# Performance work log

Measured on AMD Instinct MI355X. Metric: run time of the kernel, lower is better.

The kernel has to match this reference:

```python
import jax, jax.numpy as jnp
import numpy as np
import math

B, T, N, C = 16, 24, 207, 64
E = 16   # embedding_dim
L = 3    # num_layers
NH = 4   # temporal attention heads
HD = C // NH
HOR = 12 # horizon


def _ln(x, w, b, eps=1e-5):
    m = x.mean(-1, keepdims=True)
    v = ((x - m) ** 2).mean(-1, keepdims=True)
    return (x - m) / jnp.sqrt(v + eps) * w + b


def setup_inputs():
    ks = iter(jax.random.split(jax.random.key(0), 64))
    def g(shape, s=0.1):
        return jax.random.normal(next(ks), shape, dtype=jnp.float32) * s
    inp = {}
    inp['x'] = jax.random.normal(next(ks), (B, T, N, 4), dtype=jnp.float32)
    adj = (jax.random.uniform(next(ks), (N, N)) < 0.3).astype(jnp.float32)
    inp['static_adj'] = jnp.maximum(adj, jnp.eye(N, dtype=jnp.float32))  # self-loops: no all-zero rows
    inp['node_embedding'] = g((N, E), 1.0)
    for nm in ['hour', 'day', 'weekend']:
        inp[nm + '_w'] = g((E, 1)); inp[nm + '_b'] = g((E,))
    inp['in_w'] = g((C, 1 + 4 * E)); inp['in_b'] = g((C,))
    C8 = C // 8
    inp['sa_qw'] = g((L, C8, C)); inp['sa_qb'] = g((L, C8))
    inp['sa_kw'] = g((L, C8, C)); inp['sa_kb'] = g((L, C8))
    inp['sa_vw'] = g((L, C, C)); inp['sa_vb'] = g((L, C))
    for nm in ['ta_q', 'ta_k', 'ta_v', 'ta_o']:
        inp[nm + 'w'] = g((L, C, C)); inp[nm + 'b'] = g((L, C))
    inp['ln1_w'] = jnp.ones((L, C)); inp['ln1_b'] = jnp.zeros((L, C))
    inp['ln2_w'] = jnp.ones((L, C)); inp['ln2_b'] = jnp.zeros((L, C))
    inp['ffn_w1'] = g((L, 4 * C, C)); inp['ffn_b1'] = g((L, 4 * C))
    inp['ffn_w2'] = g((L, C, 4 * C)); inp['ffn_b2'] = g((L, C))
    inp['gru_wih'] = g((2, 3 * C, C)); inp['gru_whh'] = g((2, 3 * C, C))
    inp['gru_bih'] = g((2, 3 * C)); inp['gru_bhh'] = g((2, 3 * C))
    inp['pred_w'] = g((HOR, C * T), 0.02); inp['pred_b'] = g((HOR,))
    return inp


def _forward(x, static_adj, node_embedding, hour_w, hour_b, day_w, day_b, weekend_w, weekend_b, in_w, in_b, sa_qw, sa_qb, sa_kw, sa_kb, sa_vw, sa_vb, ta_qw, ta_qb, ta_kw, ta_kb, ta_vw, ta_vb, ta_ow, ta_ob, ln1_w, ln1_b, ln2_w, ln2_b, ffn_w1, ffn_b1, ffn_w2, ffn_b2, gru_wih, gru_whh, gru_bih, gru_bhh, pred_w, pred_b):
    # eval mode: dropout = identity, no input perturbation
    flow = x[..., :1]
    hour = x[..., 1:2]; weekend = x[..., 2:3]; day = x[..., 3:4]
    node_emb = jnp.broadcast_to(node_embedding[None, None], (B, T, N, E))
    hour_emb = hour @ hour_w.T + hour_b
    day_emb = day @ day_w.T + day_b
    weekend_emb = weekend @ weekend_w.T + weekend_b
    h = jnp.concatenate([flow, node_emb, hour_emb, day_emb, weekend_emb], axis=-1)  # [B,T,N,65]
    h = h.transpose(0, 3, 2, 1)  # [B,F,N,T]
    h = jnp.einsum('of,bfnt->bont', in_w, h) + in_b[None, :, None, None]  # 1x1 conv -> [B,C,N,T]
    # positional encoding (added along channel/time, matching permute in torch)
    pos = jnp.arange(100, dtype=jnp.float32)[:, None]
    div = jnp.exp(jnp.arange(0, C, 2, dtype=jnp.float32) * (-math.log(10000.0) / C))
    pe = jnp.stack([jnp.sin(pos * div), jnp.cos(pos * div)], axis=-1).reshape(100, C)
    h = h + pe[:T].T[None, :, None, :]
    # F.normalize(adj, p=1, dim=-1) with eps clamp (torch default 1e-12)
    adj_norm = static_adj / jnp.maximum(jnp.abs(static_adj).sum(-1, keepdims=True), 1e-12)
    zero_mask = (adj_norm == 0)[None]  # [1,N,N]
    attn_mats = []
    sqrtC = math.sqrt(C); sqrtHD = math.sqrt(HD)
    for l in range(L):
        # ---- spatial attention (faithful dim-mixing reshapes of the original) ----
        hp = h.transpose(0, 1, 3, 2)  # [B,C,T,N]
        q = jnp.einsum('oc,bctn->botn', sa_qw[l], hp) + sa_qb[l][None, :, None, None]
        k = jnp.einsum('oc,bctn->botn', sa_kw[l], hp) + sa_kb[l][None, :, None, None]
        v = jnp.einsum('oc,bctn->botn', sa_vw[l], hp) + sa_vb[l][None, :, None, None]
        C8 = q.shape[1]
        q2 = q.reshape(B * T, C8, N).transpose(0, 2, 1)
        k2 = k.reshape(B * T, C8, N)
        v2 = v.reshape(B * T, C, N)
        attn = jax.nn.softmax(jnp.einsum('bnc,bcm->bnm', q2, k2) / sqrtC, axis=-1)
        attn = jnp.where(zero_mask, -jnp.inf, attn)
        attn = jax.nn.softmax(attn, axis=-1)
        sp = jnp.einsum('bcn,bmn->bcm', v2, attn).reshape(B, T, C, N).transpose(0, 2, 3, 1)  # [B,C,N,T]
        attn_mats.append(attn.reshape(B, T, N, N))
        h = h + sp
        h = _ln(h.transpose(0, 3, 2, 1), ln1_w[l], ln1_b[l]).transpose(0, 3, 2, 1)
        # ---- temporal attention (multi-head over time, per node) ----
        xt = h.transpose(0, 2, 3, 1)  # [B,N,T,C]
        def heads(w, b):
            return (xt @ w.T + b).reshape(B, N, T, NH, HD).transpose(0, 1, 3, 2, 4)
        tq = heads(ta_qw[l], ta_qb[l]); tk = heads(ta_kw[l], ta_kb[l]); tv = heads(ta_vw[l], ta_vb[l])
        scores = jnp.einsum('bnhtd,bnhsd->bnhts', tq, tk) / sqrtHD
        ta = jnp.einsum('bnhts,bnhsd->bnhtd', jax.nn.softmax(scores, axis=-1), tv)
        ta = ta.transpose(0, 1, 3, 2, 4).reshape(B, N, T, C) @ ta_ow[l].T + ta_ob[l]
        h = h + ta.transpose(0, 3, 1, 2)
        # ---- LN2 + FFN (residual taken post-LN2, as in the original) ----
        hl = _ln(h.transpose(0, 3, 2, 1), ln2_w[l], ln2_b[l])  # [B,T,N,C]
        ffn = jax.nn.relu(hl @ ffn_w1[l].T + ffn_b1[l]) @ ffn_w2[l].T + ffn_b2[l]
        h = (hl + ffn).transpose(0, 3, 2, 1)
    # ---- 2-layer GRU over time per (batch, node) ----
    seq = h.transpose(0, 2, 3, 1).reshape(B * N, T, C).transpose(1, 0, 2)  # [T,BN,C]
    for l in range(2):
        xp = jnp.einsum('tbc,gc->tbg', seq, gru_wih[l]) + gru_bih[l]
        whh = gru_whh[l]; bhh = gru_bhh[l]
        def step(hprev, xg):
            hg = hprev @ whh.T + bhh
            r = jax.nn.sigmoid(xg[:, :C] + hg[:, :C])
            z = jax.nn.sigmoid(xg[:, C:2 * C] + hg[:, C:2 * C])
            n = jnp.tanh(xg[:, 2 * C:] + r * hg[:, 2 * C:])
            hnew = (1 - z) * n + z * hprev
            return hnew, hnew
        _, seq = jax.lax.scan(step, jnp.zeros((B * N, C), dtype=seq.dtype), xp)
    h = seq.transpose(1, 0, 2).reshape(B, N, T, C).transpose(0, 3, 1, 2)  # [B,C,N,T]
    # ---- prediction head ----
    flat = h.transpose(0, 2, 1, 3).reshape(B * N, C * T)
    out = (flat @ pred_w.T + pred_b).reshape(B, N, HOR).transpose(0, 2, 1)  # [B,HOR,N]
    return out, attn_mats


def reference(x, static_adj, node_embedding, hour_w, hour_b, day_w, day_b, weekend_w, weekend_b, in_w, in_b, sa_qw, sa_qb, sa_kw, sa_kb, sa_vw, sa_vb, ta_qw, ta_qb, ta_kw, ta_kb, ta_vw, ta_vb, ta_ow, ta_ob, ln1_w, ln1_b, ln2_w, ln2_b, ffn_w1, ffn_b1, ffn_w2, ffn_b2, gru_wih, gru_whh, gru_bih, gru_bhh, pred_w, pred_b):
    out, attn_mats = _forward(x, static_adj, node_embedding, hour_w, hour_b, day_w, day_b, weekend_w, weekend_b, in_w, in_b, sa_qw, sa_qb, sa_kw, sa_kb, sa_vw, sa_vb, ta_qw, ta_qb, ta_kw, ta_kb, ta_vw, ta_vb, ta_ow, ta_ob, ln1_w, ln1_b, ln2_w, ln2_b, ffn_w1, ffn_b1, ffn_w2, ffn_b2, gru_wih, gru_whh, gru_bih, gru_bhh, pred_w, pred_b)
    return (out, jnp.stack(attn_mats))
```

## Files before the change

### kernel.cpp

```cpp
#include <hip/hip_runtime.h>
#include <math.h>

namespace {

constexpr int B = 16, T = 24, N = 207, C = 64, HOR = 12;
constexpr int BT = B * T;
constexpr int BN = B * N;
constexpr int P = B * T * N;
constexpr int NC = N * C;

constexpr size_t H_OFF = 0;
constexpr size_t A_OFF = 5087232;
constexpr size_t Q_OFF = A_OFF + 5087232;
constexpr size_t K_OFF = Q_OFF + 635904;
constexpr size_t B_OFF = K_OFF + 635904;
constexpr size_t WS_FLOATS = B_OFF + 20348928;

__device__ __forceinline__ float wsum(float v) {
#pragma unroll
  for (int off = 32; off; off >>= 1) v += __shfl_xor(v, off);
  return v;
}
__device__ __forceinline__ float wmax(float v) {
#pragma unroll
  for (int off = 32; off; off >>= 1) v = fmaxf(v, __shfl_xor(v, off));
  return v;
}

__global__ __launch_bounds__(256) void k_embed(
    const float* __restrict__ x, const float* __restrict__ nodee,
    const float* __restrict__ hw, const float* __restrict__ hb,
    const float* __restrict__ dw, const float* __restrict__ db,
    const float* __restrict__ ww, const float* __restrict__ wb,
    const float* __restrict__ inw, const float* __restrict__ inb,
    float* __restrict__ H) {
  int pos = blockIdx.x * 4 + (threadIdx.x >> 6);
  int c = threadIdx.x & 63;
  int n = pos % N;
  int t = (pos / N) % T;
  const float* xv = x + (size_t)pos * 4;
  float flow = xv[0], hour = xv[1], wkend = xv[2], day = xv[3];
  const float* w = inw + c * 65;
  float acc = inb[c] + w[0] * flow;
#pragma unroll
  for (int e = 0; e < 16; e++) {
    acc += w[1 + e] * nodee[n * 16 + e];
    acc += w[17 + e] * (hour * hw[e] + hb[e]);
    acc += w[33 + e] * (day * dw[e] + db[e]);
    acc += w[49 + e] * (wkend * ww[e] + wb[e]);
  }
  int i = c >> 1;
  float dv = expf((float)(2 * i) * (-9.210340371976184f / 64.0f));
  float ang = (float)t * dv;
  acc += (c & 1) ? cosf(ang) : sinf(ang);
  H[(size_t)pos * 64 + c] = acc;
}

__global__ __launch_bounds__(256) void k_spatial_qkv(
    const float* __restrict__ H, const float* __restrict__ qw,
    const float* __restrict__ qb, const float* __restrict__ kw,
    const float* __restrict__ kb, const float* __restrict__ vw,
    const float* __restrict__ vb, float* __restrict__ q, float* __restrict__ k,
    float* __restrict__ v, int l) {
  __shared__ float hs[N * 65];
  int g = blockIdx.x;
  int b = g / T, t = g % T;
  const float* Hbt = H + (size_t)g * NC;
  for (int e = threadIdx.x; e < NC; e += 256) {
    int n = e >> 6, c = e & 63;
    hs[n * 65 + c] = Hbt[e];
  }
  __syncthreads();
  qw += l * 8 * 64; qb += l * 8;
  kw += l * 8 * 64; kb += l * 8;
  vw += l * 64 * 64; vb += l * 64;
  for (int e = threadIdx.x; e < 16 * N; e += 256) {
    int o = e / N, n = e % N;
    int oo = o & 7;
    const float* W = (o < 8 ? qw : kw) + oo * 64;
    float acc = (o < 8 ? qb : kb)[oo];
#pragma unroll
    for (int c = 0; c < 64; c++) acc += W[c] * hs[n * 65 + c];
    size_t oidx = ((size_t)(b * 8 + oo) * T + t) * N + n;
    if (o < 8) q[oidx] = acc; else k[oidx] = acc;
  }
  for (int e = threadIdx.x; e < 64 * N; e += 256) {
    int o = e / N, n = e % N;
    const float* W = vw + o * 64;
    float acc = vb[o];
#pragma unroll
    for (int c = 0; c < 64; c++) acc += W[c] * hs[n * 65 + c];
    v[((size_t)(b * 64 + o) * T + t) * N + n] = acc;
  }
}

__global__ __launch_bounds__(256) void k_spatial_attn(
    const float* __restrict__ q, const float* __restrict__ k,
    const float* __restrict__ adj, float* __restrict__ attn_out) {
  __shared__ float qs[8 * 208], ks[8 * 208];
  int g = blockIdx.x;
  const float* qg = q + (size_t)g * 1656;
  const float* kg = k + (size_t)g * 1656;
  for (int e = threadIdx.x; e < 1656; e += 256) {
    int c2 = e / N, n = e % N;
    qs[c2 * 208 + n] = qg[e];
    ks[c2 * 208 + n] = kg[e];
  }
  __syncthreads();
  int wave = threadIdx.x >> 6, lane = threadIdx.x & 63;
  for (int n = wave; n < N; n += 4) {
    float s[4];
    float mx = -INFINITY;
#pragma unroll
    for (int j = 0; j < 4; j++) {
      int m = lane + 64 * j;
      float acc = -INFINITY;
      if (m < N) {
        acc = 0.f;
#pragma unroll
        for (int c2 = 0; c2 < 8; c2++) acc += qs[c2 * 208 + n] * ks[c2 * 208 + m];
        acc *= 0.125f;
      }
      s[j] = acc;
      mx = fmaxf(mx, acc);
    }
    mx = wmax(mx);
    float sum = 0.f;
#pragma unroll
    for (int j = 0; j < 4; j++) {
      int m = lane + 64 * j;
      float e = (m < N) ? expf(s[j] - mx) : 0.f;
      s[j] = e;
      sum += e;
    }
    sum = wsum(sum);
    float inv = 1.f / sum;
    float mx2 = -INFINITY;
    bool ok[4];
#pragma unroll
    for (int j = 0; j < 4; j++) {
      int m = lane + 64 * j;
      float p = s[j] * inv;
      bool valid = (m < N) && (adj[n * N + m] != 0.0f);
      ok[j] = valid;
      s[j] = p;
      if (valid) mx2 = fmaxf(mx2, p);
    }
    mx2 = wmax(mx2);
    float sum2 = 0.f;
#pragma unroll
    for (int j = 0; j < 4; j++) {
      float e = ok[j] ? expf(s[j] - mx2) : 0.f;
      s[j] = e;
      sum2 += e;
    }
    sum2 = wsum(sum2);
    float inv2 = 1.f / sum2;
    float* orow = attn_out + ((size_t)g * N + n) * N;
#pragma unroll
    for (int j = 0; j < 4; j++) {
      int m = lane + 64 * j;
      if (m < N) orow[m] = s[j] * inv2;
    }
  }
}

__global__ __launch_bounds__(256, 3) void k_spatial_apply(
    const float* __restrict__ v, const float* __restrict__ attn,
    float* __restrict__ H) {
  __shared__ float vs[64 * 207];
  int g = blockIdx.x;
  int ms = blockIdx.y;
  const float* vg = v + (size_t)g * NC;
  for (int e = threadIdx.x; e < NC; e += 256) vs[e] = vg[e];
  __syncthreads();
  int wave = threadIdx.x >> 6, lane = threadIdx.x & 63;
  const float* ag = attn + (size_t)g * (N * N);
  float* Hg = H + (size_t)g * NC;
  int mbeg = ms * 52;
  int mend = min(mbeg + 52, N);
  int m_w = mbeg + wave;
  size_t Dg = (size_t)g * (N * N);
  int p = (int)((4 - ((Dg + (size_t)m_w * N) & 3)) & 3);
  const float* ar[13];
  int mrow[13];
#pragma unroll
  for (int r = 0; r < 13; r++) {
    int m = m_w + 4 * r;
    mrow[r] = m;
    int msafe = (m < N) ? m : m - 4;
    ar[r] = ag + (size_t)msafe * N;
  }
  float acc[13];
#pragma unroll
  for (int r = 0; r < 13; r++) acc[r] = 0.f;
  const float* vrow = vs + lane * 207;
  for (int n = 0; n < p; n++) {
    float vv = vrow[n];
#pragma unroll
    for (int r = 0; r < 13; r++) acc[r] += vv * ar[r][n];
  }
  for (int n4 = 0; n4 < 51; n4++) {
    int n = p + n4 * 4;
    float v0 = vrow[n], v1 = vrow[n + 1], v2 = vrow[n + 2], v3 = vrow[n + 3];
#pragma unroll
    for (int r = 0; r < 13; r++) {
      float4 a = *(const float4*)(ar[r] + n);
      acc[r] += v0 * a.x;
      acc[r] += v1 * a.y;
      acc[r] += v2 * a.z;
      acc[r] += v3 * a.w;
    }
  }
  for (int n = p + 204; n < 207; n++) {
    float vv = vrow[n];
#pragma unroll
    for (int r = 0; r < 13; r++) acc[r] += vv * ar[r][n];
  }
#pragma unroll
  for (int r = 0; r < 13; r++) {
    int m = mrow[r];
    if (m < mend) Hg[(size_t)m * 64 + lane] += acc[r];
  }
}

__global__ __launch_bounds__(256) void k_ln1(float* __restrict__ H,
                                             const float* __restrict__ w,
                                             const float* __restrict__ b, int l) {
  int pos = blockIdx.x * 4 + (threadIdx.x >> 6);
  int c = threadIdx.x & 63;
  float xv = H[(size_t)pos * 64 + c];
  float mean = wsum(xv) * (1.f / 64.f);
  float d = xv - mean;
  float var = wsum(d * d) * (1.f / 64.f);
  H[(size_t)pos * 64 + c] = d / sqrtf(var + 1e-5f) * w[l * 64 + c] + b[l * 64 + c];
}

__global__ __launch_bounds__(256) void k_temporal(
    float* __restrict__ H, const float* __restrict__ qw,
    const float* __restrict__ qb, const float* __restrict__ kw,
    const float* __restrict__ kb, const float* __restrict__ vw,
    const float* __restrict__ vb, const float* __restrict__ ow,
    const float* __restrict__ ob, int l) {
  __shared__ float xs[24 * 66], qs[24 * 66], ks[24 * 66], vs[24 * 66];
  __shared__ float ss[96 * 25];
  __shared__ float wbuf[64 * 65];
  int bn = blockIdx.x;
  int b = bn / N, n = bn % N;
  size_t base = ((size_t)b * T * N + n) * 64;
  int lane = threadIdx.x & 63, tg = threadIdx.x >> 6;
  for (int t = tg; t < 24; t += 4) xs[t * 66 + lane] = H[base + (size_t)t * NC + lane];
  const float* Wm[4] = {qw + l * 4096, kw + l * 4096, vw + l * 4096, ow + l * 4096};
  const float* Bm[4] = {qb + l * 64, kb + l * 64, vb + l * 64, ob + l * 64};
  float* Dm[3] = {qs, ks, vs};
#pragma unroll
  for (int ph = 0; ph < 3; ph++) {
    for (int e = threadIdx.x; e < 4096; e += 256)
      wbuf[(e >> 6) * 65 + (e & 63)] = Wm[ph][e];
    __syncthreads();
    float acc[6];
    float bv = Bm[ph][lane];
#pragma unroll
    for (int i = 0; i < 6; i++) acc[i] = bv;
    for (int c = 0; c < 64; c++) {
      float wv = wbuf[lane * 65 + c];
#pragma unroll
      for (int i = 0; i < 6; i++) acc[i] += wv * xs[(tg * 6 + i) * 66 + c];
    }
    float* dst = Dm[ph];
#pragma unroll
    for (int i = 0; i < 6; i++) dst[(tg * 6 + i) * 66 + lane] = acc[i];
    __syncthreads();
  }
  for (int e = threadIdx.x; e < 2304; e += 256) {
    int u = e % 24, t = (e / 24) % 24, h = e / 576;
    float a = 0.f;
#pragma unroll
    for (int d = 0; d < 16; d++)
      a += qs[t * 66 + h * 16 + d] * ks[u * 66 + h * 16 + d];
    ss[(h * 24 + t) * 25 + u] = a * 0.25f;
  }
  __syncthreads();
  if (threadIdx.x < 96) {
    float* row = ss + threadIdx.x * 25;
    float mx = -INFINITY;
#pragma unroll
    for (int u = 0; u < 24; u++) mx = fmaxf(mx, row[u]);
    float sum = 0.f;
#pragma unroll
    for (int u = 0; u < 24; u++) {
      float e2 = expf(row[u] - mx);
      row[u] = e2;
      sum += e2;
    }
    float inv = 1.f / sum;
#pragma unroll
    for (int u = 0; u < 24; u++) row[u] *= inv;
  }
  __syncthreads();
  for (int e = threadIdx.x; e < 1536; e += 256) {
    int t = e >> 6, c = e & 63, h = c >> 4;
    float a = 0.f;
#pragma unroll
    for (int u = 0; u < 24; u++) a += ss[(h * 24 + t) * 25 + u] * vs[u * 66 + c];
    xs[t * 66 + c] = a;
  }
  __syncthreads();
  for (int e = threadIdx.x; e < 4096; e += 256)
    wbuf[(e >> 6) * 65 + (e & 63)] = Wm[3][e];
  __syncthreads();
  float acc[6];
  float bv = Bm[3][lane];
#pragma unroll
  for (int i = 0; i < 6; i++) acc[i] = bv;
  for (int cp = 0; cp < 64; cp++) {
    float wv = wbuf[lane * 65 + cp];
#pragma unroll
    for (int i = 0; i < 6; i++) acc[i] += wv * xs[(tg * 6 + i) * 66 + cp];
  }
#pragma unroll
  for (int i = 0; i < 6; i++)
    H[base + (size_t)(tg * 6 + i) * NC + lane] += acc[i];
}

__global__ __launch_bounds__(256) void k_transpose_ffn(
    const float* __restrict__ w1, const float* __restrict__ w2,
    float* __restrict__ w1t, float* __restrict__ w2q, int l) {
  int e = blockIdx.x * 256 + threadIdx.x;
  if (e < 16384) {
    int c = e >> 8, j = e & 255;
    w1t[e] = w1[l * 16384 + j * 64 + c];
  } else {
    int m = e - 16384;
    int jq = m >> 8, c = (m & 255) >> 2, kk = m & 3;
    w2q[m] = w2[l * 16384 + c * 256 + jq * 4 + kk];
  }
}

__global__ __launch_bounds__(256) void k_ffn(
    float* __restrict__ H, const float* __restrict__ lnw,
    const float* __restrict__ lnb, const float* __restrict__ w1t,
    const float* __restrict__ b1, const float* __restrict__ w2q,
    const float* __restrict__ b2, int l) {
  __shared__ float xs[24 * 66];
  __shared__ float hids[24 * 260];
  int bn = blockIdx.x;
  int b = bn / N, n = bn % N;
  size_t base = ((size_t)b * T * N + n) * 64;
  int lane = threadIdx.x & 63, tg = threadIdx.x >> 6;
  for (int t = tg; t < 24; t += 4) {
    float xv = H[base + (size_t)t * NC + lane];
    float mean = wsum(xv) * (1.f / 64.f);
    float d = xv - mean;
    float var = wsum(d * d) * (1.f / 64.f);
    xs[t * 66 + lane] = d / sqrtf(var + 1e-5f) * lnw[l * 64 + lane] + lnb[l * 64 + lane];
  }
  __syncthreads();
  int j0 = lane * 4;
  float4 b4 = *(const float4*)(b1 + l * 256 + j0);
  float a0[6], a1[6], a2[6], a3[6];
#pragma unroll
  for (int i = 0; i < 6; i++) { a0[i] = b4.x; a1[i] = b4.y; a2[i] = b4.z; a3[i] = b4.w; }
  for (int c = 0; c < 64; c++) {
    float4 w4 = *(const float4*)(w1t + c * 256 + j0);
#pragma unroll
    for (int i = 0; i < 6; i++) {
      float xv = xs[(tg * 6 + i) * 66 + c];
      a0[i] += xv * w4.x;
      a1[i] += xv * w4.y;
      a2[i] += xv * w4.z;
      a3[i] += xv * w4.w;
    }
  }
#pragma unroll
  for (int i = 0; i < 6; i++) {
    int t = tg * 6 + i;
    float4 r = make_float4(fmaxf(a0[i], 0.f), fmaxf(a1[i], 0.f),
                           fmaxf(a2[i], 0.f), fmaxf(a3[i], 0.f));
    *(float4*)(&hids[t * 260 + j0]) = r;
  }
  __syncthreads();
  const float4* w2q4 = (const float4*)w2q;
  float acc[6];
#pragma unroll
  for (int i = 0; i < 6; i++) acc[i] = 0.f;
  for (int jq = 0; jq < 64; jq++) {
    float4 w = w2q4[jq * 64 + lane];
#pragma unroll
    for (int i = 0; i < 6; i++) {
      float4 hv = *(const float4*)(&hids[(tg * 6 + i) * 260 + jq * 4]);
      acc[i] += hv.x * w.x + hv.y * w.y + hv.z * w.z + hv.w * w.w;
    }
  }
  float bias = b2[l * 64 + lane];
#pragma unroll
  for (int i = 0; i < 6; i++) {
    int t = tg * 6 + i;
    H[base + (size_t)t * NC + lane] = xs[t * 66 + lane] + bias + acc[i];
  }
}

__global__ __launch_bounds__(256) void k_gru_xp(
    const float* __restrict__ X, const float* __restrict__ wih,
    const float* __restrict__ bih, float* __restrict__ xp, int l) {
  __shared__ float ws_[192 * 65];
  __shared__ float xv[16 * 64];
  int p0 = blockIdx.x * 16;
  for (int e = threadIdx.x; e < 192 * 64; e += 256) {
    int gI = e >> 6, c = e & 63;
    ws_[gI * 65 + c] = wih[l * 12288 + e];
  }
  for (int e = threadIdx.x; e < 16 * 64; e += 256) {
    int s = e >> 6, c = e & 63;
    int p = p0 + s;
    int t = p / BN, bn = p % BN;
    float val;
    if (l == 0) {
      int b = bn / N, n = bn % N;
      val = X[(((size_t)b * T + t) * N + n) * 64 + c];
    } else {
      val = X[(size_t)p * 64 + c];
    }
    xv[e] = val;
  }
  __syncthreads();
  for (int e = threadIdx.x; e < 16 * 192; e += 256) {
    int s = e / 192, gI = e % 192;
    float acc = bih[l * 192 + gI];
#pragma unroll
    for (int c = 0; c < 64; c++) acc += xv[s * 64 + c] * ws_[gI * 65 + c];
    xp[((size_t)(p0 + s)) * 192 + gI] = acc;
  }
}

__global__ __launch_bounds__(256) void k_gru_scan(
    const float* __restrict__ xp, const float* __restrict__ whh,
    const float* __restrict__ bhh, float* __restrict__ seq_out, int l) {
  constexpr int S = 8;
  __shared__ float hprev[S][64];
  __shared__ float hg[3][S][64];
  __shared__ float xpbuf[2][S * 192];
  int bn0 = blockIdx.x * S;
  int lane = threadIdx.x & 63;
  int wv = threadIdx.x >> 6;

  float4 w4[16];
  if (wv < 3) {
    const float* wr = whh + l * 12288 + (wv * 64 + lane) * 64;
#pragma unroll
    for (int j = 0; j < 16; j++) w4[j] = *(const float4*)(wr + j * 4);
  }
  float b_r = bhh[l * 192 + lane];
  float b_z = bhh[l * 192 + 64 + lane];
  float b_n = bhh[l * 192 + 128 + lane];

  for (int e = threadIdx.x; e < S * 64; e += 256) ((float*)hprev)[e] = 0.f;
  {
    const float* src = xp + (size_t)bn0 * 192;
    for (int e = threadIdx.x; e < S * 192; e += 256) xpbuf[0][e] = src[e];
  }
  __syncthreads();

  for (int t = 0; t < T; t++) {
    int cur = t & 1;
    if (wv < 3) {
      float acc[S];
#pragma unroll
      for (int s = 0; s < S; s++) acc[s] = 0.f;
#pragma unroll
      for (int j = 0; j < 16; j++) {
        float4 w = w4[j];
#pragma unroll
        for (int s = 0; s < S; s++) {
          float4 hb = *(const float4*)(&hprev[s][j * 4]);
          acc[s] += w.x * hb.x + w.y * hb.y + w.z * hb.z + w.w * hb.w;
        }
      }
#pragma unroll
      for (int s = 0; s < S; s++) hg[wv][s][lane] = acc[s];
    } else {
      if (t + 1 < T) {
        const float* src = xp + ((size_t)(t + 1) * BN + bn0) * 192;
        float* dst = xpbuf[(t + 1) & 1];
        for (int e = lane * 4; e < S * 192; e += 256) {
          *(float4*)(dst + e) = *(const float4*)(src + e);
        }
      }
    }
    __syncthreads();
#pragma unroll
    for (int ii = 0; ii < 2; ii++) {
      int s = wv + 4 * ii;
      const float* xr = &xpbuf[cur][s * 192];
      float r = 1.f / (1.f + expf(-(xr[lane] + hg[0][s][lane] + b_r)));
      float z = 1.f / (1.f + expf(-(xr[64 + lane] + hg[1][s][lane] + b_z)));
      float nn = tanhf(xr[128 + lane] + r * (hg[2][s][lane] + b_n));
      float hp = hprev[s][lane];
      float hnew = (1.f - z) * nn + z * hp;
      hprev[s][lane] = hnew;
      seq_out[((size_t)t * BN + bn0 + s) * 64 + lane] = hnew;
    }
    __syncthreads();
  }
}

__global__ __launch_bounds__(256) void k_pred(
    const float* __restrict__ seq2, const float* __restrict__ pw,
    const float* __restrict__ pb, float* __restrict__ out) {
  __shared__ float s_[1536];
  int bn = blockIdx.x;
  int b = bn / N, n = bn % N;
  for (int e = threadIdx.x; e < 1536; e += 256) {
    int t = e >> 6, c = e & 63;
    s_[c * 24 + t] = seq2[((size_t)t * BN + bn) * 64 + c];
  }
  __syncthreads();
  int wave = threadIdx.x >> 6, lane = threadIdx.x & 63;
  for (int hor = wave; hor < 12; hor += 4) {
    const float* w = pw + hor * 1536;
    float acc = 0.f;
#pragma unroll 4
    for (int kk = lane; kk < 1536; kk += 64) acc += s_[kk] * w[kk];
    acc = wsum(acc);
    if (lane == 0) out[(size_t)b * (HOR * N) + hor * N + n] = acc + pb[hor];
  }
}

}

extern "C" void kernel_launch(void* const* d_in, const int* in_sizes, int n_in,
                              void* d_out, int out_size, void* d_ws, size_t ws_size,
                              hipStream_t stream) {
  const float* x       = (const float*)d_in[0];
  const float* adj     = (const float*)d_in[1];
  const float* nodee   = (const float*)d_in[2];
  const float* hour_w  = (const float*)d_in[3];
  const float* hour_b  = (const float*)d_in[4];
  const float* day_w   = (const float*)d_in[5];
  const float* day_b   = (const float*)d_in[6];
  const float* wk_w    = (const float*)d_in[7];
  const float* wk_b    = (const float*)d_in[8];
  const float* in_w    = (const float*)d_in[9];
  const float* in_b    = (const float*)d_in[10];
  const float* sa_qw   = (const float*)d_in[11];
  const float* sa_qb   = (const float*)d_in[12];
  const float* sa_kw   = (const float*)d_in[13];
  const float* sa_kb   = (const float*)d_in[14];
  const float* sa_vw   = (const float*)d_in[15];
  const float* sa_vb   = (const float*)d_in[16];
  const float* ta_qw   = (const float*)d_in[17];
  const float* ta_qb   = (const float*)d_in[18];
  const float* ta_kw   = (const float*)d_in[19];
  const float* ta_kb   = (const float*)d_in[20];
  const float* ta_vw   = (const float*)d_in[21];
  const float* ta_vb   = (const float*)d_in[22];
  const float* ta_ow   = (const float*)d_in[23];
  const float* ta_ob   = (const float*)d_in[24];
  const float* ln1_w   = (const float*)d_in[25];
  const float* ln1_b   = (const float*)d_in[26];
  const float* ln2_w   = (const float*)d_in[27];
  const float* ln2_b   = (const float*)d_in[28];
  const float* ffn_w1  = (const float*)d_in[29];
  const float* ffn_b1  = (const float*)d_in[30];
  const float* ffn_w2  = (const float*)d_in[31];
  const float* ffn_b2  = (const float*)d_in[32];
  const float* gru_wih = (const float*)d_in[33];
  const float* gru_whh = (const float*)d_in[34];
  const float* gru_bih = (const float*)d_in[35];
  const float* gru_bhh = (const float*)d_in[36];
  const float* pred_w  = (const float*)d_in[37];
  const float* pred_b  = (const float*)d_in[38];

  if (ws_size < WS_FLOATS * sizeof(float)) return;

  float* ws   = (float*)d_ws;
  float* H    = ws + H_OFF;
  float* bufA = ws + A_OFF;
  float* q    = ws + Q_OFF;
  float* k    = ws + K_OFF;
  float* bufB = ws + B_OFF;

  float* out       = (float*)d_out;
  float* attn_base = out + (size_t)B * HOR * N;

  float* v   = bufB;
  float* xp  = bufB;
  float* w1t = q;
  float* w2q = k;

  k_embed<<<P / 4, 256, 0, stream>>>(x, nodee, hour_w, hour_b, day_w, day_b,
                                     wk_w, wk_b, in_w, in_b, H);

  for (int l = 0; l < 3; l++) {
    float* attn_l = attn_base + (size_t)l * BT * N * N;
    k_spatial_qkv<<<BT, 256, 0, stream>>>(H, sa_qw, sa_qb, sa_kw, sa_kb, sa_vw,
                                          sa_vb, q, k, v, l);
    k_spatial_attn<<<BT, 256, 0, stream>>>(q, k, adj, attn_l);
    k_spatial_apply<<<dim3(BT, 4), 256, 0, stream>>>(v, attn_l, H);
    k_ln1<<<P / 4, 256, 0, stream>>>(H, ln1_w, ln1_b, l);
    k_temporal<<<BN, 256, 0, stream>>>(H, ta_qw, ta_qb, ta_kw, ta_kb, ta_vw,
                                       ta_vb, ta_ow, ta_ob, l);
    k_transpose_ffn<<<128, 256, 0, stream>>>(ffn_w1, ffn_w2, w1t, w2q, l);
    k_ffn<<<BN, 256, 0, stream>>>(H, ln2_w, ln2_b, w1t, ffn_b1, w2q, ffn_b2, l);
  }

  k_gru_xp<<<P / 16, 256, 0, stream>>>(H, gru_wih, gru_bih, xp, 0);
  k_gru_scan<<<BN / 8, 256, 0, stream>>>(xp, gru_whh, gru_bhh, bufA, 0);
  k_gru_xp<<<P / 16, 256, 0, stream>>>(bufA, gru_wih, gru_bih, xp, 1);
  k_gru_scan<<<BN / 8, 256, 0, stream>>>(xp, gru_whh, gru_bhh, H, 1);

  k_pred<<<BN, 256, 0, stream>>>(H, pred_w, pred_b, out);
}
```

Measured before the change: 2.397 ms.

## Fuse LayerNorm1 into temporal attention and read pre-packed weights from global

```diff
diff --git a/kernel.cpp b/kernel.cpp
--- a/kernel.cpp
+++ b/kernel.cpp
@@ -224,60 +224,59 @@
   }
 }
 
-__global__ __launch_bounds__(256) void k_ln1(float* __restrict__ H,
-                                             const float* __restrict__ w,
-                                             const float* __restrict__ b, int l) {
-  int pos = blockIdx.x * 4 + (threadIdx.x >> 6);
-  int c = threadIdx.x & 63;
-  float xv = H[(size_t)pos * 64 + c];
-  float mean = wsum(xv) * (1.f / 64.f);
-  float d = xv - mean;
-  float var = wsum(d * d) * (1.f / 64.f);
-  H[(size_t)pos * 64 + c] = d / sqrtf(var + 1e-5f) * w[l * 64 + c] + b[l * 64 + c];
-}
-
 __global__ __launch_bounds__(256) void k_temporal(
-    float* __restrict__ H, const float* __restrict__ qw,
-    const float* __restrict__ qb, const float* __restrict__ kw,
-    const float* __restrict__ kb, const float* __restrict__ vw,
-    const float* __restrict__ vb, const float* __restrict__ ow,
-    const float* __restrict__ ob, int l) {
-  __shared__ float xs[24 * 66], qs[24 * 66], ks[24 * 66], vs[24 * 66];
+    float* __restrict__ H, const float* __restrict__ taq,
+    const float* __restrict__ qb, const float* __restrict__ kb,
+    const float* __restrict__ vb, const float* __restrict__ ob,
+    const float* __restrict__ lnw, const float* __restrict__ lnb, int l) {
+  __shared__ float xs[24 * 68], qs[24 * 68], ks[24 * 68], vs[24 * 68];
   __shared__ float ss[96 * 25];
-  __shared__ float wbuf[64 * 65];
   int bn = blockIdx.x;
   int b = bn / N, n = bn % N;
   size_t base = ((size_t)b * T * N + n) * 64;
   int lane = threadIdx.x & 63, tg = threadIdx.x >> 6;
-  for (int t = tg; t < 24; t += 4) xs[t * 66 + lane] = H[base + (size_t)t * NC + lane];
-  const float* Wm[4] = {qw + l * 4096, kw + l * 4096, vw + l * 4096, ow + l * 4096};
-  const float* Bm[4] = {qb + l * 64, kb + l * 64, vb + l * 64, ob + l * 64};
+  float lw = lnw[l * 64 + lane], lb = lnb[l * 64 + lane];
+  for (int t = tg; t < 24; t += 4) {
+    float xv = H[base + (size_t)t * NC + lane];
+    float mean = wsum(xv) * (1.f / 64.f);
+    float d = xv - mean;
+    float var = wsum(d * d) * (1.f / 64.f);
+    xs[t * 68 + lane] = d / sqrtf(var + 1e-5f) * lw + lb;
+  }
+  __syncthreads();
+  const float4* wq_all = (const float4*)taq;
+  const float* Bm[3] = {qb + l * 64, kb + l * 64, vb + l * 64};
   float* Dm[3] = {qs, ks, vs};
 #pragma unroll
   for (int ph = 0; ph < 3; ph++) {
-    for (int e = threadIdx.x; e < 4096; e += 256)
-      wbuf[(e >> 6) * 65 + (e & 63)] = Wm[ph][e];
-    __syncthreads();
+    const float4* wq = wq_all + ph * 1024;
     float acc[6];
     float bv = Bm[ph][lane];
 #pragma unroll
     for (int i = 0; i < 6; i++) acc[i] = bv;
-    for (int c = 0; c < 64; c++) {
-      float wv = wbuf[lane * 65 + c];
-#pragma unroll
-      for (int i = 0; i < 6; i++) acc[i] += wv * xs[(tg * 6 + i) * 66 + c];
+#pragma unroll 4
+    for (int cq = 0; cq < 16; cq++) {
+      float4 w = wq[cq * 64 + lane];
+#pragma unroll
+      for (int i = 0; i < 6; i++) {
+        float4 xv = *(const float4*)(&xs[(tg * 6 + i) * 68 + cq * 4]);
+        acc[i] += xv.x * w.x + xv.y * w.y + xv.z * w.z + xv.w * w.w;
+      }
     }
     float* dst = Dm[ph];
 #pragma unroll
-    for (int i = 0; i < 6; i++) dst[(tg * 6 + i) * 66 + lane] = acc[i];
-    __syncthreads();
-  }
+    for (int i = 0; i < 6; i++) dst[(tg * 6 + i) * 68 + lane] = acc[i];
+  }
+  __syncthreads();
   for (int e = threadIdx.x; e < 2304; e += 256) {
     int u = e % 24, t = (e / 24) % 24, h = e / 576;
     float a = 0.f;
 #pragma unroll
-    for (int d = 0; d < 16; d++)
-      a += qs[t * 66 + h * 16 + d] * ks[u * 66 + h * 16 + d];
+    for (int dq = 0; dq < 4; dq++) {
+      float4 qv = *(const float4*)(&qs[t * 68 + h * 16 + dq * 4]);
+      float4 kv = *(const float4*)(&ks[u * 68 + h * 16 + dq * 4]);
+      a += qv.x * kv.x + qv.y * kv.y + qv.z * kv.z + qv.w * kv.w;
+    }
     ss[(h * 24 + t) * 25 + u] = a * 0.25f;
   }
   __syncthreads();
@@ -298,42 +297,65 @@
     for (int u = 0; u < 24; u++) row[u] *= inv;
   }
   __syncthreads();
-  for (int e = threadIdx.x; e < 1536; e += 256) {
-    int t = e >> 6, c = e & 63, h = c >> 4;
-    float a = 0.f;
-#pragma unroll
-    for (int u = 0; u < 24; u++) a += ss[(h * 24 + t) * 25 + u] * vs[u * 66 + c];
-    xs[t * 66 + c] = a;
-  }
-  __syncthreads();
-  for (int e = threadIdx.x; e < 4096; e += 256)
-    wbuf[(e >> 6) * 65 + (e & 63)] = Wm[3][e];
-  __syncthreads();
-  float acc[6];
-  float bv = Bm[3][lane];
-#pragma unroll
-  for (int i = 0; i < 6; i++) acc[i] = bv;
-  for (int cp = 0; cp < 64; cp++) {
-    float wv = wbuf[lane * 65 + cp];
-#pragma unroll
-    for (int i = 0; i < 6; i++) acc[i] += wv * xs[(tg * 6 + i) * 66 + cp];
-  }
-#pragma unroll
-  for (int i = 0; i < 6; i++)
-    H[base + (size_t)(tg * 6 + i) * NC + lane] += acc[i];
-}
-
-__global__ __launch_bounds__(256) void k_transpose_ffn(
+  {
+    int h = lane >> 4;
+    float acc2[6];
+#pragma unroll
+    for (int i = 0; i < 6; i++) acc2[i] = 0.f;
+    for (int u = 0; u < 24; u++) {
+      float vsv = vs[u * 68 + lane];
+#pragma unroll
+      for (int i = 0; i < 6; i++)
+        acc2[i] += ss[(h * 24 + (tg * 6 + i)) * 25 + u] * vsv;
+    }
+#pragma unroll
+    for (int i = 0; i < 6; i++) qs[(tg * 6 + i) * 68 + lane] = acc2[i];
+  }
+  __syncthreads();
+  {
+    const float4* wo = wq_all + 3 * 1024;
+    float acc[6];
+    float bv = ob[l * 64 + lane];
+#pragma unroll
+    for (int i = 0; i < 6; i++) acc[i] = bv;
+#pragma unroll 4
+    for (int cq = 0; cq < 16; cq++) {
+      float4 w = wo[cq * 64 + lane];
+#pragma unroll
+      for (int i = 0; i < 6; i++) {
+        float4 xv = *(const float4*)(&qs[(tg * 6 + i) * 68 + cq * 4]);
+        acc[i] += xv.x * w.x + xv.y * w.y + xv.z * w.z + xv.w * w.w;
+      }
+    }
+#pragma unroll
+    for (int i = 0; i < 6; i++)
+      H[base + (size_t)(tg * 6 + i) * NC + lane] =
+          xs[(tg * 6 + i) * 68 + lane] + acc[i];
+  }
+}
+
+__global__ __launch_bounds__(256) void k_pack(
     const float* __restrict__ w1, const float* __restrict__ w2,
-    float* __restrict__ w1t, float* __restrict__ w2q, int l) {
+    const float* __restrict__ tqw, const float* __restrict__ tkw,
+    const float* __restrict__ tvw, const float* __restrict__ tow,
+    float* __restrict__ w1t, float* __restrict__ w2q, float* __restrict__ taq,
+    int l) {
   int e = blockIdx.x * 256 + threadIdx.x;
   if (e < 16384) {
     int c = e >> 8, j = e & 255;
     w1t[e] = w1[l * 16384 + j * 64 + c];
-  } else {
+  } else if (e < 32768) {
     int m = e - 16384;
     int jq = m >> 8, c = (m & 255) >> 2, kk = m & 3;
     w2q[m] = w2[l * 16384 + c * 256 + jq * 4 + kk];
+  } else {
+    int m2 = e - 32768;
+    int ph = m2 >> 12;
+    int m = m2 & 4095;
+    int cq = m >> 8, o = (m & 255) >> 2, j = m & 3;
+    const float* src =
+        (ph == 0 ? tqw : ph == 1 ? tkw : ph == 2 ? tvw : tow) + l * 4096;
+    taq[ph * 4096 + m] = src[o * 64 + 4 * cq + j];
   }
 }
 
@@ -587,6 +609,7 @@
   float* xp  = bufB;
   float* w1t = q;
   float* w2q = k;
+  float* taq = bufA;
 
   k_embed<<<P / 4, 256, 0, stream>>>(x, nodee, hour_w, hour_b, day_w, day_b,
                                      wk_w, wk_b, in_w, in_b, H);
@@ -596,11 +619,11 @@
     k_spatial_qkv<<<BT, 256, 0, stream>>>(H, sa_qw, sa_qb, sa_kw, sa_kb, sa_vw,
                                           sa_vb, q, k, v, l);
     k_spatial_attn<<<BT, 256, 0, stream>>>(q, k, adj, attn_l);
+    k_pack<<<192, 256, 0, stream>>>(ffn_w1, ffn_w2, ta_qw, ta_kw, ta_vw, ta_ow,
+                                    w1t, w2q, taq, l);
     k_spatial_apply<<<dim3(BT, 4), 256, 0, stream>>>(v, attn_l, H);
-    k_ln1<<<P / 4, 256, 0, stream>>>(H, ln1_w, ln1_b, l);
-    k_temporal<<<BN, 256, 0, stream>>>(H, ta_qw, ta_qb, ta_kw, ta_kb, ta_vw,
-                                       ta_vb, ta_ow, ta_ob, l);
-    k_transpose_ffn<<<128, 256, 0, stream>>>(ffn_w1, ffn_w2, w1t, w2q, l);
+    k_temporal<<<BN, 256, 0, stream>>>(H, taq, ta_qb, ta_kb, ta_vb, ta_ob,
+                                       ln1_w, ln1_b, l);
     k_ffn<<<BN, 256, 0, stream>>>(H, ln2_w, ln2_b, w1t, ffn_b1, w2q, ffn_b2, l);
   }
 
```

After: 2.277 ms. -5.0%, faster.
